# Kernel tuning notes

Measured on AMD Instinct MI355X. Metric: run time of the kernel, lower is better.

Reference implementation:

```python
import jax, jax.numpy as jnp
import numpy as np

N, E, G, H = 5000, 50000, 8, 4
GAT_DIMS = [(1536, 1024), (1024, 512), (512, 256)]
MLP_DIMS = [(256, 128), (128, 64), (64, 32), (32, 16), (16, 1)]
GATE_DIMS = [(256, 128), (128, 1)]
NEG_SLOPE = 0.2
EPS = 1e-16


def setup_inputs() -> dict:
    key = jax.random.key(0)
    keys = iter(jax.random.split(key, 80))

    def nrm(shape, s=0.05):
        return jax.random.normal(next(keys), shape, jnp.float32) * s

    inp = {}
    inp["x"] = jax.random.normal(next(keys), (N, 1536), jnp.float32)
    inp["edge_index"] = jax.random.randint(next(keys), (2, E), 0, N)
    inp["batch"] = jnp.sort(jax.random.randint(next(keys), (N,), 0, G))
    for i, (di, do) in enumerate(GAT_DIMS, 1):
        inp[f"Wl{i}"] = nrm((di, H * do))
        inp[f"bl{i}"] = jnp.zeros((H * do,), jnp.float32)
        inp[f"Wr{i}"] = nrm((di, H * do))
        inp[f"br{i}"] = jnp.zeros((H * do,), jnp.float32)
        inp[f"att{i}"] = nrm((H, do))
        inp[f"b{i}"] = jnp.zeros((do,), jnp.float32)
    for i, (di, do) in enumerate(MLP_DIMS):
        inp[f"Wm{i}"] = nrm((di, do))
        inp[f"bm{i}"] = jnp.zeros((do,), jnp.float32)
    for i, (di, do) in enumerate(GATE_DIMS):
        inp[f"Wg{i}"] = nrm((di, do))
        inp[f"bg{i}"] = jnp.zeros((do,), jnp.float32)
    return inp


def _gatv2(x, src, dst, Wl, bl, Wr, br, att, bias):
    # PyG GATv2Conv, concat=False: mean over heads.
    C = att.shape[1]
    xl = (x @ Wl + bl).reshape(-1, H, C)  # source-side transform [N,H,C]
    xr = (x @ Wr + br).reshape(-1, H, C)  # target-side transform [N,H,C]
    # edge scores: att . leaky_relu(x_j + x_i)  -> [E',H]
    s = jnp.sum(jax.nn.leaky_relu(xl[src] + xr[dst], negative_slope=NEG_SLOPE) * att, axis=-1)
    # segment softmax over destination node neighborhoods
    m = jax.ops.segment_max(s, dst, num_segments=N)
    ex = jnp.exp(s - m[dst])
    den = jax.ops.segment_sum(ex, dst, num_segments=N)
    alpha = ex / (den[dst] + EPS)
    out = jax.ops.segment_sum(alpha[:, :, None] * xl[src], dst, num_segments=N)  # [N,H,C]
    return out.mean(axis=1) + bias


def _forward(x, edge_index, batch, params):
    loop = jnp.arange(N)
    src = jnp.concatenate([edge_index[0], loop])  # add_self_loops=True (PyG default)
    dst = jnp.concatenate([edge_index[1], loop])
    for i in (1, 2, 3):
        x = jax.nn.relu(_gatv2(x, src, dst,
                               params[f"Wl{i}"], params[f"bl{i}"],
                               params[f"Wr{i}"], params[f"br{i}"],
                               params[f"att{i}"], params[f"b{i}"]))
    # AttentionalAggregation: segment-softmax(gate_nn(x)) weighted sum over graphs
    gate = jax.nn.relu(x @ params["Wg0"] + params["bg0"]) @ params["Wg1"] + params["bg1"]
    g = gate[:, 0]
    m = jax.ops.segment_max(g, batch, num_segments=G)
    ex = jnp.exp(g - m[batch])
    den = jax.ops.segment_sum(ex, batch, num_segments=G)
    w = ex / (den[batch] + EPS)
    h = jax.ops.segment_sum(w[:, None] * x, batch, num_segments=G)  # [G,256]
    for i in range(4):
        h = jax.nn.relu(h @ params[f"Wm{i}"] + params[f"bm{i}"])
    return h @ params["Wm4"] + params["bm4"]  # [G,1]


def reference(x, edge_index, batch,
              Wl1, bl1, Wr1, br1, att1, b1,
              Wl2, bl2, Wr2, br2, att2, b2,
              Wl3, bl3, Wr3, br3, att3, b3,
              Wm0, bm0, Wm1, bm1, Wm2, bm2, Wm3, bm3, Wm4, bm4,
              Wg0, bg0, Wg1, bg1):
    params = dict(locals())
    for k in ("x", "edge_index", "batch"):
        params.pop(k)
    return _forward(x, edge_index, batch, params)
```

## Files before the change

### kernel.cpp

```cpp
#include <hip/hip_runtime.h>
#include <math.h>

#define NN 5000
#define NNP 5120
#define NE 50000
#define NEE 55000
#define NG 8
#define NH 4

typedef __attribute__((ext_vector_type(8))) _Float16 half8;
typedef __attribute__((ext_vector_type(4))) _Float16 half4;
typedef __attribute__((ext_vector_type(4))) float floatx4;


__device__ inline float waveSum(float v) {
    #pragma unroll
    for (int o = 32; o > 0; o >>= 1) v += __shfl_xor(v, o, 64);
    return v;
}
__device__ inline float waveMax(float v) {
    #pragma unroll
    for (int o = 32; o > 0; o >>= 1) v = fmaxf(v, __shfl_xor(v, o, 64));
    return v;
}

__device__ __forceinline__ void gload_lds16(const _Float16* g, _Float16* l) {
    __builtin_amdgcn_global_load_lds(
        (__attribute__((address_space(1))) void*)g,
        (__attribute__((address_space(3))) void*)l,
        16, 0, 0);
}

template<int N>
__device__ __forceinline__ void vmgate() {
    if constexpr (N == 0) asm volatile("s_waitcnt vmcnt(0)" ::: "memory");
    else if constexpr (N == 2) asm volatile("s_waitcnt vmcnt(2)" ::: "memory");
    else if constexpr (N == 4) asm volatile("s_waitcnt vmcnt(4)" ::: "memory");
}


__global__ void k_cvtA(const float* __restrict__ X, _Float16* __restrict__ A0, int n) {
    int i = blockIdx.x * 256 + threadIdx.x;
    if (i >= n) return;
    A0[i] = (_Float16)X[i];
}

__global__ __launch_bounds__(256) void k_cvtWT(const float* __restrict__ W,
        _Float16* __restrict__ B0, int K, int M)
{
    __shared__ float tile[32][33];
    int m0 = blockIdx.x * 32, k0 = blockIdx.y * 32;
    int tx = threadIdx.x & 31, ty = threadIdx.x >> 5;
    #pragma unroll
    for (int i = 0; i < 4; ++i)
        tile[ty + 8 * i][tx] = W[(size_t)(k0 + ty + 8 * i) * M + m0 + tx];
    __syncthreads();
    #pragma unroll
    for (int i = 0; i < 4; ++i) {
        int mm = ty + 8 * i, kk = tx;
        B0[(size_t)(m0 + mm) * K + kk + k0] = (_Float16)tile[kk][mm];
    }
}

__global__ __launch_bounds__(512, 2) void gemm256_mfma_f16(
    const _Float16* __restrict__ A0, const _Float16* __restrict__ B0,
    const float* __restrict__ biasL, const float* __restrict__ biasR,
    int Nhalf, _Float16* __restrict__ C,
    int Mrows, int K, int N)
{
    __shared__ __align__(16) _Float16 smem[2 * 32768];

    const int tid  = threadIdx.x;
    const int wave = tid >> 6;
    const int lane = tid & 63;
    const int wr = wave >> 2;
    const int wc = wave & 3;
    const int rowBase = blockIdx.y * 256;
    const int colBase = blockIdx.x * 256;

    floatx4 acc[2][2][4][2];
    #pragma unroll
    for (int qa = 0; qa < 2; ++qa)
        #pragma unroll
        for (int qb = 0; qb < 2; ++qb)
            #pragma unroll
            for (int f = 0; f < 4; ++f)
                #pragma unroll
                for (int g = 0; g < 2; ++g)
                    acc[qa][qb][f][g] = (floatx4){0.f, 0.f, 0.f, 0.f};

    const int srow   = lane >> 3;
    const int schunk = ((lane & 7) ^ srow) << 3;
    const _Float16* gA = A0 + (size_t)(rowBase + wave * 16 + srow) * K + schunk;
    const _Float16* gB = B0 + (size_t)(colBase + wave * 16 + srow) * K + schunk;
    const size_t rstep = (size_t)8 * K;
    const size_t hstep = (size_t)128 * K;

    auto stageA = [&](int b, int h, int kt) {
        _Float16* l = &smem[b * 32768 + (h * 128 + wave * 16) * 64];
        const _Float16* g = gA + (size_t)h * hstep + (size_t)kt * 64;
        gload_lds16(g, l);
        gload_lds16(g + rstep, l + 512);
    };
    auto stageB = [&](int b, int h, int kt) {
        _Float16* l = &smem[b * 32768 + 16384 + (h * 128 + wave * 16) * 64];
        const _Float16* g = gB + (size_t)h * hstep + (size_t)kt * 64;
        gload_lds16(g, l);
        gload_lds16(g + rstep, l + 512);
    };

    auto phase = [&](auto qa_c, auto qb_c, auto gate_c, const _Float16* Ab,
                     const _Float16* Bb, auto stg) {
        constexpr int QA = decltype(qa_c)::value;
        constexpr int QB = decltype(qb_c)::value;
        constexpr int GATE = decltype(gate_c)::value;
        const int lm = lane & 15;
        const int key = lane & 7;
        const int kg = lane >> 4;
        half8 af[4][2], bf[2][2];
        #pragma unroll
        for (int f = 0; f < 4; ++f)
            #pragma unroll
            for (int s = 0; s < 2; ++s) {
                int row = QA * 128 + wr * 64 + f * 16 + lm;
                int ch = (s * 4 + kg) ^ key;
                af[f][s] = *(const half8*)&Ab[row * 64 + ch * 8];
            }
        #pragma unroll
        for (int g = 0; g < 2; ++g)
            #pragma unroll
            for (int s = 0; s < 2; ++s) {
                int row = QB * 128 + wc * 32 + g * 16 + lm;
                int ch = (s * 4 + kg) ^ key;
                bf[g][s] = *(const half8*)&Bb[row * 64 + ch * 8];
            }
        stg();
        __builtin_amdgcn_s_barrier();
        __builtin_amdgcn_s_setprio(1);
        #pragma unroll
        for (int f = 0; f < 4; ++f)
            #pragma unroll
            for (int g = 0; g < 2; ++g)
                #pragma unroll
                for (int s = 0; s < 2; ++s)
                    acc[QA][QB][f][g] = __builtin_amdgcn_mfma_f32_16x16x32_f16(
                        af[f][s], bf[g][s], acc[QA][QB][f][g], 0, 0, 0);
        __builtin_amdgcn_s_setprio(0);
        vmgate<GATE>();
        __builtin_amdgcn_s_barrier();
        __builtin_amdgcn_sched_barrier(0);
    };

    auto ic = [](auto v) { return v; };
    using i0 = std::integral_constant<int, 0>;
    using i1 = std::integral_constant<int, 1>;
    using gN = std::integral_constant<int, -1>;
    using g0 = std::integral_constant<int, 0>;
    using g2 = std::integral_constant<int, 2>;
    using g4 = std::integral_constant<int, 4>;
    (void)ic;

    stageA(0, 0, 0); stageA(0, 1, 0); stageB(0, 0, 0); stageB(0, 1, 0);
    vmgate<2>();
    __builtin_amdgcn_s_barrier();

    const int nk = K >> 6;
    for (int t = 0; t < nk - 1; ++t) {
        const int b = t & 1;
        const _Float16* Ab = &smem[b * 32768];
        const _Float16* Bb = Ab + 16384;
        phase(i0{}, i0{}, gN{}, Ab, Bb, [&]{ stageA(b ^ 1, 0, t + 1); });
        phase(i1{}, i0{}, g4{}, Ab, Bb, [&]{ stageA(b ^ 1, 1, t + 1); });
        phase(i0{}, i1{}, gN{}, Ab, Bb, [&]{ stageB(b ^ 1, 0, t + 1); });
        phase(i1{}, i1{}, g2{}, Ab, Bb, [&]{ stageB(b ^ 1, 1, t + 1); });
    }
    {
        const int b = (nk - 1) & 1;
        const _Float16* Ab = &smem[b * 32768];
        const _Float16* Bb = Ab + 16384;
        phase(i0{}, i0{}, gN{}, Ab, Bb, [&]{});
        phase(i1{}, i0{}, g0{}, Ab, Bb, [&]{});
        phase(i0{}, i1{}, gN{}, Ab, Bb, [&]{});
        phase(i1{}, i1{}, gN{}, Ab, Bb, [&]{});
    }

    _Float16* Ct = smem;
    const int lm = lane & 15;
    const int cq = (lane >> 4) * 4;
    #pragma unroll
    for (int qb = 0; qb < 2; ++qb)
        #pragma unroll
        for (int g = 0; g < 2; ++g) {
            int col = qb * 128 + wc * 32 + g * 16 + lm;
            int gcol = colBase + col;
            float bv = (gcol < Nhalf) ? biasL[gcol] : biasR[gcol - Nhalf];
            #pragma unroll
            for (int qa = 0; qa < 2; ++qa)
                #pragma unroll
                for (int f = 0; f < 4; ++f)
                    #pragma unroll
                    for (int r = 0; r < 4; ++r) {
                        int row = qa * 128 + wr * 64 + f * 16 + cq + r;
                        int gi = (col >> 4) ^ ((row >> 2) & 7);
                        Ct[row * 256 + gi * 16 + (col & 15)] =
                            (_Float16)(acc[qa][qb][f][g][r] + bv);
                    }
        }
    __syncthreads();
    const int r0 = tid >> 5;
    const int cc = (tid & 31) * 8;
    const int gg = cc >> 4;
    #pragma unroll
    for (int ps = 0; ps < 16; ++ps) {
        int row = ps * 16 + r0;
        int grow = rowBase + row;
        if (grow < Mrows) {
            int gp = gg ^ ((row >> 2) & 7);
            half8 v = *(const half8*)&Ct[row * 256 + gp * 16 + (cc & 15)];
            *(half8*)&C[(size_t)grow * N + colBase + cc] = v;
        }
    }
}

__global__ __launch_bounds__(256) void gemm_mfma_f16(
    const _Float16* __restrict__ A0, const _Float16* __restrict__ B0,
    const float* __restrict__ biasL, const float* __restrict__ biasR,
    int Nhalf, _Float16* __restrict__ C,
    int Mrows, int K, int N)
{
    __shared__ __align__(16) _Float16 smem[2 * 2 * 128 * 32];
    _Float16* As = smem;
    _Float16* Bs = smem + 2 * 128 * 32;

    const int tid = threadIdx.x;
    const int wave = tid >> 6;
    const int lane = tid & 63;
    const int wm = (wave >> 1) * 64;
    const int wn = (wave & 1) * 64;
    const int lm = lane & 15;
    const int swz = (((lane >> 4) ^ ((lane >> 1) & 3)) << 3);

    const int rowBase = blockIdx.y * 128;
    const int colBase = blockIdx.x * 128;

    floatx4 acc[4][4];
    #pragma unroll
    for (int i = 0; i < 4; ++i)
        #pragma unroll
        for (int j = 0; j < 4; ++j)
            acc[i][j] = (floatx4){0.f, 0.f, 0.f, 0.f};

    const int sr = lane >> 2;
    const int scol = (((lane & 3) ^ ((lane >> 3) & 3)) << 3);
    const _Float16* gA = A0 + (size_t)(rowBase + wave * 32 + sr) * K + scol;
    const _Float16* gB = B0 + (size_t)(colBase + wave * 32 + sr) * K + scol;
    const size_t skip16 = (size_t)16 * K;
    const int lo0 = (wave * 32) * 32;
    const int lo1 = (wave * 32 + 16) * 32;

    gload_lds16(gA, &As[lo0]);
    gload_lds16(gA + skip16, &As[lo1]);
    gload_lds16(gB, &Bs[lo0]);
    gload_lds16(gB + skip16, &Bs[lo1]);
    __syncthreads();

    const int nk = K >> 5;
    for (int t = 0; t < nk; ++t) {
        const int p = t & 1;
        const int po = p * 128 * 32;
        if (t + 1 < nk) {
            const int k1 = (t + 1) << 5;
            const int qo = (p ^ 1) * 128 * 32;
            gload_lds16(gA + k1, &As[qo + lo0]);
            gload_lds16(gA + skip16 + k1, &As[qo + lo1]);
            gload_lds16(gB + k1, &Bs[qo + lo0]);
            gload_lds16(gB + skip16 + k1, &Bs[qo + lo1]);
        }
        half8 a0[4], b0[4];
        #pragma unroll
        for (int i = 0; i < 4; ++i) {
            a0[i] = *(const half8*)&As[po + (wm + i * 16 + lm) * 32 + swz];
            b0[i] = *(const half8*)&Bs[po + (wn + i * 16 + lm) * 32 + swz];
        }
        #pragma unroll
        for (int i = 0; i < 4; ++i)
            #pragma unroll
            for (int j = 0; j < 4; ++j)
                acc[i][j] = __builtin_amdgcn_mfma_f32_16x16x32_f16(a0[i], b0[j], acc[i][j], 0, 0, 0);
        __syncthreads();
    }

    _Float16* Ct = smem;
    const int cq = (lane >> 4) * 4;
    #pragma unroll
    for (int j = 0; j < 4; ++j) {
        int col = wn + j * 16 + lm;
        int gcol = colBase + col;
        float bv = (gcol < Nhalf) ? biasL[gcol] : biasR[gcol - Nhalf];
        #pragma unroll
        for (int i = 0; i < 4; ++i) {
            int row = wm + i * 16 + cq;
            #pragma unroll
            for (int r = 0; r < 4; ++r) {
                int rr = row + r;
                Ct[rr * 128 + (col ^ (((rr >> 2) & 7) << 4))] = (_Float16)(acc[i][j][r] + bv);
            }
        }
    }
    __syncthreads();
    const int r0 = tid >> 4;
    const int cc = (tid & 15) * 8;
    #pragma unroll
    for (int ps = 0; ps < 8; ++ps) {
        int row = ps * 16 + r0;
        int grow = rowBase + row;
        if (grow < Mrows) {
            half8 v = *(const half8*)&Ct[row * 128 + (cc ^ (((row >> 2) & 7) << 4))];
            *(half8*)&C[(size_t)grow * N + colBase + cc] = v;
        }
    }
}


__global__ void k_build_edges(const int* __restrict__ ei, int* __restrict__ src,
                              int* __restrict__ dst) {
    int i = blockIdx.x * 256 + threadIdx.x;
    if (i < NE) { src[i] = ei[i]; dst[i] = ei[NE + i]; }
    else if (i < NEE) { src[i] = i - NE; dst[i] = i - NE; }
}

__global__ void k_zero32(unsigned int* __restrict__ p, int n) {
    int i = blockIdx.x * 256 + threadIdx.x;
    if (i < n) p[i] = 0u;
}

__global__ void k_count(const int* __restrict__ dst, int* __restrict__ cnt) {
    int i = blockIdx.x * 256 + threadIdx.x;
    if (i < NEE) atomicAdd(&cnt[dst[i]], 1);
}

__global__ __launch_bounds__(256) void k_scan(const int* __restrict__ cnt,
                                              int* __restrict__ off, int* __restrict__ cur) {
    __shared__ int partial[256];
    __shared__ int ppre[257];
    int t = threadIdx.x;
    const int chunk = (NN + 255) / 256;
    int lo = t * chunk, hi = min(NN, (t + 1) * chunk);
    int s = 0;
    for (int i = lo; i < hi; ++i) s += cnt[i];
    partial[t] = s;
    __syncthreads();
    if (t == 0) {
        int acc = 0;
        for (int i = 0; i < 256; ++i) { ppre[i] = acc; acc += partial[i]; }
        ppre[256] = acc;
    }
    __syncthreads();
    int acc = ppre[t];
    for (int i = lo; i < hi; ++i) { off[i] = acc; cur[i] = acc; acc += cnt[i]; }
    if (t == 0) off[NN] = ppre[256];
}

__global__ void k_fill(const int* __restrict__ src, const int* __restrict__ dst,
                       int* __restrict__ cur, int* __restrict__ slist) {
    int e = blockIdx.x * 256 + threadIdx.x;
    if (e < NEE) { int p = atomicAdd(&cur[dst[e]], 1); slist[p] = src[e]; }
}

template<int C>
__global__ __launch_bounds__(256) void k_gat_fused(
    const _Float16* __restrict__ xlr, const float* __restrict__ att,
    const int* __restrict__ eoff, const int* __restrict__ slist,
    const float* __restrict__ bias, _Float16* __restrict__ out)
{
    constexpr int LD = 2 * NH * C;
    constexpr int CH = (C >= 512) ? 8 : 4;
    constexpr int NC = C / (64 * CH);
    constexpr int PL = NC * CH;
    __shared__ float red[NH * C];
    const int n = blockIdx.x;
    const int h = threadIdx.x >> 6;
    const int lane = threadIdx.x & 63;

    float xrv[PL], attv[PL], acc[PL];
    {
        const _Float16* xrrow = xlr + (size_t)n * LD + NH * C + h * C + lane * CH;
        const float* ah = att + h * C + lane * CH;
        #pragma unroll
        for (int c = 0; c < NC; ++c) {
            if constexpr (CH == 8) {
                half8 hv = *(const half8*)(xrrow + c * 64 * CH);
                #pragma unroll
                for (int e = 0; e < 8; ++e) xrv[c * 8 + e] = (float)hv[e];
            } else {
                half4 hv = *(const half4*)(xrrow + c * 64 * CH);
                #pragma unroll
                for (int e = 0; e < 4; ++e) xrv[c * 4 + e] = (float)hv[e];
            }
            #pragma unroll
            for (int e = 0; e < CH; e += 4) {
                float4 a4 = *(const float4*)(ah + c * 64 * CH + e);
                attv[c * CH + e + 0] = a4.x; attv[c * CH + e + 1] = a4.y;
                attv[c * CH + e + 2] = a4.z; attv[c * CH + e + 3] = a4.w;
            }
        }
        #pragma unroll
        for (int e = 0; e < PL; ++e) acc[e] = 0.f;
    }

    float m = -INFINITY, den = 0.f;
    const int start = eoff[n], end = eoff[n + 1];

    _Float16 bufA[PL], bufB[PL];
    auto ldrow = [&](int s, _Float16* buf) {
        const _Float16* p = xlr + (size_t)s * LD + h * C + lane * CH;
        #pragma unroll
        for (int c = 0; c < NC; ++c) {
            if constexpr (CH == 8)
                *(half8*)&buf[c * 8] = *(const half8*)(p + c * 64 * CH);
            else
                *(half4*)&buf[c * 4] = *(const half4*)(p + c * 64 * CH);
        }
    };

    if (start < end) ldrow(slist[start], bufA);
    for (int j = start; j < end; ++j) {
        if (j + 1 < end) ldrow(slist[j + 1], bufB);
        float xv[PL];
        float ps = 0.f;
        #pragma unroll
        for (int e = 0; e < PL; ++e) {
            xv[e] = (float)bufA[e];
            float v = xv[e] + xrv[e];
            v = v > 0.f ? v : 0.2f * v;
            ps = fmaf(v, attv[e], ps);
        }
        ps = waveSum(ps);
        float m_new = fmaxf(m, ps);
        float scale = expf(m - m_new);
        float ex = expf(ps - m_new);
        den = den * scale + ex;
        m = m_new;
        #pragma unroll
        for (int e = 0; e < PL; ++e)
            acc[e] = fmaf(ex, xv[e], acc[e] * scale);
        #pragma unroll
        for (int e = 0; e < PL; ++e) bufA[e] = bufB[e];
    }

    float inv = 1.f / (den + 1e-16f);
    #pragma unroll
    for (int c = 0; c < NC; ++c) {
        int off = h * C + c * 64 * CH + lane * CH;
        #pragma unroll
        for (int e = 0; e < CH; e += 4) {
            float4 r;
            r.x = acc[c * CH + e + 0] * inv;
            r.y = acc[c * CH + e + 1] * inv;
            r.z = acc[c * CH + e + 2] * inv;
            r.w = acc[c * CH + e + 3] * inv;
            *(float4*)&red[off + e] = r;
        }
    }
    __syncthreads();

    int t = threadIdx.x;
    for (int c4 = t; c4 < C / 4; c4 += 256) {
        int c = c4 * 4;
        float4 r0 = *(const float4*)&red[0 * C + c];
        float4 r1 = *(const float4*)&red[1 * C + c];
        float4 r2 = *(const float4*)&red[2 * C + c];
        float4 r3 = *(const float4*)&red[3 * C + c];
        float4 bv = *(const float4*)(bias + c);
        half4 o;
        o[0] = (_Float16)fmaxf((r0.x + r1.x + r2.x + r3.x) * 0.25f + bv.x, 0.f);
        o[1] = (_Float16)fmaxf((r0.y + r1.y + r2.y + r3.y) * 0.25f + bv.y, 0.f);
        o[2] = (_Float16)fmaxf((r0.z + r1.z + r2.z + r3.z) * 0.25f + bv.z, 0.f);
        o[3] = (_Float16)fmaxf((r0.w + r1.w + r2.w + r3.w) * 0.25f + bv.w, 0.f);
        *(half4*)(out + (size_t)n * C + c) = o;
    }
}


__global__ __launch_bounds__(128) void k_gate(
    const _Float16* __restrict__ x, const float* __restrict__ Wg0,
    const float* __restrict__ bg0, const float* __restrict__ Wg1,
    const float* __restrict__ bg1, float* __restrict__ g)
{
    int n = blockIdx.x;
    int t = threadIdx.x;
    __shared__ float xs[256];
    __shared__ float wsum[2];
    const _Float16* xp = x + (size_t)n * 256;
    xs[t] = (float)xp[t]; xs[t + 128] = (float)xp[t + 128];
    __syncthreads();
    float acc = bg0[t];
    for (int k = 0; k < 256; ++k) acc = fmaf(xs[k], Wg0[k * 128 + t], acc);
    acc = acc > 0.f ? acc : 0.f;
    float prod = acc * Wg1[t];
    prod = waveSum(prod);
    if ((t & 63) == 0) wsum[t >> 6] = prod;
    __syncthreads();
    if (t == 0) g[n] = wsum[0] + wsum[1] + bg1[0];
}

__global__ void k_group_bounds(const int* __restrict__ batch, int* __restrict__ gstart,
                               int* __restrict__ gend) {
    int n = blockIdx.x * 256 + threadIdx.x;
    if (n >= NN) return;
    int b = batch[n];
    if (n == 0 || batch[n - 1] != b) gstart[b] = n;
    if (n == NN - 1 || batch[n + 1] != b) gend[b] = n + 1;
}

__global__ __launch_bounds__(256) void k_pool_stats(
    const float* __restrict__ g, const int* __restrict__ gstart,
    const int* __restrict__ gend, float* __restrict__ mOut,
    float* __restrict__ invdenOut)
{
    int gi = blockIdx.x;
    int t = threadIdx.x;
    int s0 = gstart[gi], e0 = gend[gi];
    __shared__ float red[4];
    float mx = -1e30f;
    for (int n = s0 + t; n < e0; n += 256) mx = fmaxf(mx, g[n]);
    float wm = waveMax(mx);
    if ((t & 63) == 0) red[t >> 6] = wm;
    __syncthreads();
    float m = fmaxf(fmaxf(red[0], red[1]), fmaxf(red[2], red[3]));
    __syncthreads();
    float sm = 0.f;
    for (int n = s0 + t; n < e0; n += 256) sm += expf(g[n] - m);
    sm = waveSum(sm);
    if ((t & 63) == 0) red[t >> 6] = sm;
    __syncthreads();
    if (t == 0) {
        float den = red[0] + red[1] + red[2] + red[3] + 1e-16f;
        mOut[gi] = m;
        invdenOut[gi] = 1.f / den;
    }
}

#define PCH 16
__global__ __launch_bounds__(256) void k_pool_acc(
    const _Float16* __restrict__ x, const float* __restrict__ g,
    const int* __restrict__ batch, const float* __restrict__ m,
    const float* __restrict__ invden, float* __restrict__ hpool)
{
    int base = blockIdx.x * PCH;
    int t = threadIdx.x;
    float acc = 0.f;
    int cur = -1;
    for (int i = 0; i < PCH; ++i) {
        int n = base + i;
        if (n >= NN) break;
        int b = batch[n];
        if (b != cur) {
            if (cur >= 0) atomicAdd(&hpool[cur * 256 + t], acc);
            cur = b; acc = 0.f;
        }
        float w = expf(g[n] - m[b]) * invden[b];
        acc = fmaf(w, (float)x[(size_t)n * 256 + t], acc);
    }
    if (cur >= 0) atomicAdd(&hpool[cur * 256 + t], acc);
}

__global__ __launch_bounds__(256) void k_mlp(
    const float* __restrict__ hpool,
    const float* __restrict__ Wm0, const float* __restrict__ bm0,
    const float* __restrict__ Wm1, const float* __restrict__ bm1,
    const float* __restrict__ Wm2, const float* __restrict__ bm2,
    const float* __restrict__ Wm3, const float* __restrict__ bm3,
    const float* __restrict__ Wm4, const float* __restrict__ bm4,
    float* __restrict__ out)
{
    __shared__ float bufA[8 * 256];
    __shared__ float bufB[8 * 128];
    int t = threadIdx.x;
    for (int i = t; i < 8 * 256; i += 256) bufA[i] = hpool[i];
    __syncthreads();
    for (int i = t; i < 8 * 128; i += 256) {
        int r = i >> 7, c = i & 127;
        float acc = bm0[c];
        for (int k = 0; k < 256; ++k) acc = fmaf(bufA[r * 256 + k], Wm0[k * 128 + c], acc);
        bufB[i] = fmaxf(acc, 0.f);
    }
    __syncthreads();
    for (int i = t; i < 8 * 64; i += 256) {
        int r = i >> 6, c = i & 63;
        float acc = bm1[c];
        for (int k = 0; k < 128; ++k) acc = fmaf(bufB[r * 128 + k], Wm1[k * 64 + c], acc);
        bufA[i] = fmaxf(acc, 0.f);
    }
    __syncthreads();
    for (int i = t; i < 8 * 32; i += 256) {
        int r = i >> 5, c = i & 31;
        float acc = bm2[c];
        for (int k = 0; k < 64; ++k) acc = fmaf(bufA[r * 64 + k], Wm2[k * 32 + c], acc);
        bufB[i] = fmaxf(acc, 0.f);
    }
    __syncthreads();
    for (int i = t; i < 8 * 16; i += 256) {
        int r = i >> 4, c = i & 15;
        float acc = bm3[c];
        for (int k = 0; k < 32; ++k) acc = fmaf(bufB[r * 32 + k], Wm3[k * 16 + c], acc);
        bufA[i] = fmaxf(acc, 0.f);
    }
    __syncthreads();
    if (t < 8) {
        float acc = bm4[0];
        for (int k = 0; k < 16; ++k) acc = fmaf(bufA[t * 16 + k], Wm4[k], acc);
        out[t] = acc;
    }
}


static void run_gat_layer(const _Float16* ain, int K, int C,
                          const float* Wl, const float* bl,
                          const float* Wr, const float* br,
                          const float* att, const float* bias,
                          _Float16* wb0, _Float16* xlr,
                          const int* eoff, const int* slist,
                          _Float16* xout, hipStream_t stream)
{
    int HC = NH * C;
    dim3 tgrid(HC / 32, K / 32);
    k_cvtWT<<<tgrid, 256, 0, stream>>>(Wl, wb0, K, HC);
    k_cvtWT<<<tgrid, 256, 0, stream>>>(Wr, wb0 + (size_t)HC * K, K, HC);
    if (C >= 512) {
        dim3 ggrid(2 * HC / 256, NNP / 256);
        gemm256_mfma_f16<<<ggrid, 512, 0, stream>>>(ain, wb0, bl, br, HC, xlr, NN, K, 2 * HC);
    } else {
        dim3 ggrid(2 * HC / 128, NNP / 128);
        gemm_mfma_f16<<<ggrid, 256, 0, stream>>>(ain, wb0, bl, br, HC, xlr, NN, K, 2 * HC);
    }

    if (C == 1024)
        k_gat_fused<1024><<<NN, 256, 0, stream>>>(xlr, att, eoff, slist, bias, xout);
    else if (C == 512)
        k_gat_fused<512><<<NN, 256, 0, stream>>>(xlr, att, eoff, slist, bias, xout);
    else
        k_gat_fused<256><<<NN, 256, 0, stream>>>(xlr, att, eoff, slist, bias, xout);
}

extern "C" void kernel_launch(void* const* d_in, const int* in_sizes, int n_in,
                              void* d_out, int out_size, void* d_ws, size_t ws_size,
                              hipStream_t stream) {
    const float* x      = (const float*)d_in[0];
    const int* ei       = (const int*)d_in[1];
    const int* batch    = (const int*)d_in[2];
    const float* Wl1 = (const float*)d_in[3];  const float* bl1 = (const float*)d_in[4];
    const float* Wr1 = (const float*)d_in[5];  const float* br1 = (const float*)d_in[6];
    const float* att1= (const float*)d_in[7];  const float* b1  = (const float*)d_in[8];
    const float* Wl2 = (const float*)d_in[9];  const float* bl2 = (const float*)d_in[10];
    const float* Wr2 = (const float*)d_in[11]; const float* br2 = (const float*)d_in[12];
    const float* att2= (const float*)d_in[13]; const float* b2  = (const float*)d_in[14];
    const float* Wl3 = (const float*)d_in[15]; const float* bl3 = (const float*)d_in[16];
    const float* Wr3 = (const float*)d_in[17]; const float* br3 = (const float*)d_in[18];
    const float* att3= (const float*)d_in[19]; const float* b3  = (const float*)d_in[20];
    const float* Wm0 = (const float*)d_in[21]; const float* bm0 = (const float*)d_in[22];
    const float* Wm1 = (const float*)d_in[23]; const float* bm1 = (const float*)d_in[24];
    const float* Wm2 = (const float*)d_in[25]; const float* bm2 = (const float*)d_in[26];
    const float* Wm3 = (const float*)d_in[27]; const float* bm3 = (const float*)d_in[28];
    const float* Wm4 = (const float*)d_in[29]; const float* bm4 = (const float*)d_in[30];
    const float* Wg0 = (const float*)d_in[31]; const float* bg0 = (const float*)d_in[32];
    const float* Wg1 = (const float*)d_in[33]; const float* bg1 = (const float*)d_in[34];
    float* out = (float*)d_out;

    float* ws = (float*)d_ws;
    size_t o = 0;
    _Float16* xlr = (_Float16*)(ws + o); o += (size_t)NNP * 8192 / 2;
    _Float16* x1  = (_Float16*)(ws + o); o += (size_t)NNP * 1024 / 2;
    _Float16* x2  = (_Float16*)(ws + o); o += (size_t)NNP * 512 / 2;
    _Float16* x3  = (_Float16*)(ws + o); o += (size_t)NNP * 256 / 2;
    _Float16* a0p = (_Float16*)(ws + o); o += (size_t)NNP * 1536 / 2;
    _Float16* wb0 = (_Float16*)(ws + o); o += (size_t)8192 * 1536 / 2;
    int* srcA    = (int*)(ws + o); o += NEE;
    int* dstA    = (int*)(ws + o); o += NEE;
    int* cnt     = (int*)(ws + o); o += NN;
    int* eoff    = (int*)(ws + o); o += NN + 1;
    int* cur     = (int*)(ws + o); o += NN;
    int* slist   = (int*)(ws + o); o += NEE;
    float* g     = ws + o; o += NN;
    int* gstart  = (int*)(ws + o); o += NG;
    int* gend    = (int*)(ws + o); o += NG;
    float* gm    = ws + o; o += NG;
    float* ginv  = ws + o; o += NG;
    float* hpool = ws + o; o += NG * 256;

    int ebB = (NEE + 255) / 256;
    k_build_edges<<<ebB, 256, 0, stream>>>(ei, srcA, dstA);
    k_zero32<<<(NN + 255) / 256, 256, 0, stream>>>((unsigned int*)cnt, NN);
    k_count<<<ebB, 256, 0, stream>>>(dstA, cnt);
    k_scan<<<1, 256, 0, stream>>>(cnt, eoff, cur);
    k_fill<<<ebB, 256, 0, stream>>>(srcA, dstA, cur, slist);

    int nA = NN * 1536;
    k_cvtA<<<(nA + 255) / 256, 256, 0, stream>>>(x, a0p, nA);

    run_gat_layer(a0p, 1536, 1024, Wl1, bl1, Wr1, br1, att1, b1,
                  wb0, xlr, eoff, slist, x1, stream);
    run_gat_layer(x1,  1024, 512,  Wl2, bl2, Wr2, br2, att2, b2,
                  wb0, xlr, eoff, slist, x2, stream);
    run_gat_layer(x2,  512,  256,  Wl3, bl3, Wr3, br3, att3, b3,
                  wb0, xlr, eoff, slist, x3, stream);

    k_gate<<<NN, 128, 0, stream>>>(x3, Wg0, bg0, Wg1, bg1, g);
    k_zero32<<<1, 64, 0, stream>>>((unsigned int*)gstart, 2 * NG);
    k_group_bounds<<<(NN + 255) / 256, 256, 0, stream>>>(batch, gstart, gend);
    k_pool_stats<<<NG, 256, 0, stream>>>(g, gstart, gend, gm, ginv);
    k_zero32<<<(NG * 256 + 255) / 256, 256, 0, stream>>>((unsigned int*)hpool, NG * 256);
    k_pool_acc<<<(NN + PCH - 1) / PCH, 256, 0, stream>>>(x3, g, batch, gm, ginv, hpool);
    k_mlp<<<1, 256, 0, stream>>>(hpool, Wm0, bm0, Wm1, bm1, Wm2, bm2,
                                 Wm3, bm3, Wm4, bm4, out);
}
```

Baseline: 695.6 us.

## Reuse LDS fragments across GEMM quadrant phases with reordered staging and gates

The GEMM main loop now keeps the B fragments for both column halves in registers (bf0, bf1) and reuses the A fragments across phases. Each k-step then reads fewer LDS fragments than the earlier scheme, which reloaded A and B for every quadrant. The order of phases, global-to-LDS staging and vmcnt gates is rearranged to match, including a skipped gate in one phase. This costs extra registers and a more delicate synchronisation schedule, with some risk of LDS hazards or lower occupancy.

```diff
diff --git a/kernel.cpp b/kernel.cpp
--- a/kernel.cpp
+++ b/kernel.cpp
@@ -1,5 +1,6 @@
 #include <hip/hip_runtime.h>
 #include <math.h>
+#include <type_traits>
 
 #define NN 5000
 #define NNP 5120
@@ -109,15 +110,15 @@
         gload_lds16(g + rstep, l + 512);
     };
 
-    auto phase = [&](auto qa_c, auto qb_c, auto gate_c, const _Float16* Ab,
-                     const _Float16* Bb, auto stg) {
-        constexpr int QA = decltype(qa_c)::value;
-        constexpr int QB = decltype(qb_c)::value;
-        constexpr int GATE = decltype(gate_c)::value;
-        const int lm = lane & 15;
-        const int key = lane & 7;
-        const int kg = lane >> 4;
-        half8 af[4][2], bf[2][2];
+    const int lm  = lane & 15;
+    const int key = lane & 7;
+    const int kg  = lane >> 4;
+
+    half8 af[4][2];
+    half8 bf0[2][2];
+    half8 bf1[2][2];
+
+    auto readA = [&](const _Float16* Ab, int QA) {
         #pragma unroll
         for (int f = 0; f < 4; ++f)
             #pragma unroll
@@ -126,6 +127,8 @@
                 int ch = (s * 4 + kg) ^ key;
                 af[f][s] = *(const half8*)&Ab[row * 64 + ch * 8];
             }
+    };
+    auto readB = [&](const _Float16* Bb, int QB, half8 (&bf)[2][2]) {
         #pragma unroll
         for (int g = 0; g < 2; ++g)
             #pragma unroll
@@ -134,8 +137,12 @@
                 int ch = (s * 4 + kg) ^ key;
                 bf[g][s] = *(const half8*)&Bb[row * 64 + ch * 8];
             }
-        stg();
-        __builtin_amdgcn_s_barrier();
+    };
+    constexpr std::integral_constant<int, 0> I0{};
+    constexpr std::integral_constant<int, 1> I1{};
+    auto mfma16 = [&](auto QAc, auto QBc, half8 (&bf)[2][2]) {
+        constexpr int QA = decltype(QAc)::value;
+        constexpr int QB = decltype(QBc)::value;
         __builtin_amdgcn_s_setprio(1);
         #pragma unroll
         for (int f = 0; f < 4; ++f)
@@ -146,22 +153,10 @@
                     acc[QA][QB][f][g] = __builtin_amdgcn_mfma_f32_16x16x32_f16(
                         af[f][s], bf[g][s], acc[QA][QB][f][g], 0, 0, 0);
         __builtin_amdgcn_s_setprio(0);
-        vmgate<GATE>();
-        __builtin_amdgcn_s_barrier();
-        __builtin_amdgcn_sched_barrier(0);
     };
 
-    auto ic = [](auto v) { return v; };
-    using i0 = std::integral_constant<int, 0>;
-    using i1 = std::integral_constant<int, 1>;
-    using gN = std::integral_constant<int, -1>;
-    using g0 = std::integral_constant<int, 0>;
-    using g2 = std::integral_constant<int, 2>;
-    using g4 = std::integral_constant<int, 4>;
-    (void)ic;
-
-    stageA(0, 0, 0); stageA(0, 1, 0); stageB(0, 0, 0); stageB(0, 1, 0);
-    vmgate<2>();
+    stageA(0, 0, 0); stageB(0, 0, 0); stageB(0, 1, 0); stageA(0, 1, 0);
+    vmgate<4>();
     __builtin_amdgcn_s_barrier();
 
     const int nk = K >> 6;
@@ -169,23 +164,56 @@
         const int b = t & 1;
         const _Float16* Ab = &smem[b * 32768];
         const _Float16* Bb = Ab + 16384;
-        phase(i0{}, i0{}, gN{}, Ab, Bb, [&]{ stageA(b ^ 1, 0, t + 1); });
-        phase(i1{}, i0{}, g4{}, Ab, Bb, [&]{ stageA(b ^ 1, 1, t + 1); });
-        phase(i0{}, i1{}, gN{}, Ab, Bb, [&]{ stageB(b ^ 1, 0, t + 1); });
-        phase(i1{}, i1{}, g2{}, Ab, Bb, [&]{ stageB(b ^ 1, 1, t + 1); });
+        readA(Ab, 0); readB(Bb, 0, bf0);
+        stageA(b ^ 1, 0, t + 1);
+        __builtin_amdgcn_s_barrier();
+        mfma16(I0, I0, bf0);
+        vmgate<4>();
+        __builtin_amdgcn_s_barrier();
+        __builtin_amdgcn_sched_barrier(0);
+        readB(Bb, 1, bf1);
+        stageB(b ^ 1, 0, t + 1);
+        __builtin_amdgcn_s_barrier();
+        mfma16(I0, I1, bf1);
+        vmgate<4>();
+        __builtin_amdgcn_s_barrier();
+        __builtin_amdgcn_sched_barrier(0);
+        readA(Ab, 1);
+        stageB(b ^ 1, 1, t + 1);
+        __builtin_amdgcn_s_barrier();
+        mfma16(I1, I0, bf0);
+        __builtin_amdgcn_s_barrier();
+        __builtin_amdgcn_sched_barrier(0);
+        stageA(b ^ 1, 1, t + 1);
+        __builtin_amdgcn_s_barrier();
+        mfma16(I1, I1, bf1);
+        vmgate<4>();
+        __builtin_amdgcn_s_barrier();
+        __builtin_amdgcn_sched_barrier(0);
     }
     {
         const int b = (nk - 1) & 1;
         const _Float16* Ab = &smem[b * 32768];
         const _Float16* Bb = Ab + 16384;
-        phase(i0{}, i0{}, gN{}, Ab, Bb, [&]{});
-        phase(i1{}, i0{}, g0{}, Ab, Bb, [&]{});
-        phase(i0{}, i1{}, gN{}, Ab, Bb, [&]{});
-        phase(i1{}, i1{}, gN{}, Ab, Bb, [&]{});
+        readA(Ab, 0); readB(Bb, 0, bf0);
+        __builtin_amdgcn_s_barrier();
+        mfma16(I0, I0, bf0);
+        vmgate<2>();
+        __builtin_amdgcn_s_barrier();
+        readB(Bb, 1, bf1);
+        __builtin_amdgcn_s_barrier();
+        mfma16(I0, I1, bf1);
+        vmgate<0>();
+        __builtin_amdgcn_s_barrier();
+        readA(Ab, 1);
+        __builtin_amdgcn_s_barrier();
+        mfma16(I1, I0, bf0);
+        __builtin_amdgcn_s_barrier();
+        mfma16(I1, I1, bf1);
+        __builtin_amdgcn_s_barrier();
     }
 
     _Float16* Ct = smem;
-    const int lm = lane & 15;
     const int cq = (lane >> 4) * 4;
     #pragma unroll
     for (int qb = 0; qb < 2; ++qb)
```

After: 668.2 us. 3.9% less time.
